# Optimization experiments

Hardware: AMD Instinct MI355X
Metric: run time of the kernel (lower is better)

## Reference

```python
import jax, jax.numpy as jnp
import numpy as np

B, L, D = 8, 8192, 256
H = 4 * D
EPS_LN = 1e-5
EPS_RELU = 1e-6
MIN_A, MAX_A, OFFSET = 0, 3, 3


def setup_inputs() -> dict:
    key = jax.random.key(0)
    ks = jax.random.split(key, 6)
    def n(k, shape, s=0.02):
        return jax.random.normal(k, shape, jnp.float32) * s
    return {
        "x": jax.random.normal(ks[0], (B, L, D), jnp.float32),
        "g1": jnp.ones((D,), jnp.float32), "b1": jnp.zeros((D,), jnp.float32),
        "g2": jnp.ones((D,), jnp.float32), "b2": jnp.zeros((D,), jnp.float32),
        "filt_w": n(ks[1], (L, D)),
        "w1": n(ks[2], (D, H)), "bb1": jnp.zeros((H,), jnp.float32),
        "w2": n(ks[3], (H, D)), "bb2": jnp.zeros((D,), jnp.float32),
    }


def layernorm(x, g, b):
    m = jnp.mean(x, -1, keepdims=True)
    v = jnp.var(x, -1, keepdims=True)
    return (x - m) * jax.lax.rsqrt(v + EPS_LN) * g + b


def maxpool_same(x, w):
    # stride-1 max pool over the last (frequency) axis, SAME padding
    if w == 1:
        return x
    return jax.lax.reduce_window(x, -jnp.inf, jax.lax.max,
                                 (1, 1, w), (1, 1, 1), "SAME")


def spsd1d(xt):
    """SPSD1D: FFT-based multi-scale (alpha) max-pooling spectral filter.
    xt: (B, D, L). Keeps rfft bins that are local maxima at every scale
    2**alpha for alpha in [MIN_A, MAX_A]; the lowest OFFSET bins pass through.
    Returns filtered signal (B, D, L) and argmax-alpha holder (B, D, F)."""
    X = jnp.fft.rfft(xt, axis=-1)              # (B, D, F), F = L//2 + 1
    mag = jnp.abs(X)
    pooled = jnp.stack([maxpool_same(mag, 2 ** a)
                        for a in range(MIN_A, MAX_A + 1)], 0)  # (A, B, D, F)
    max_holder = jnp.argmax(pooled, axis=0)
    env = jnp.max(pooled, axis=0)
    keep = (mag >= env) | (jnp.arange(mag.shape[-1]) < OFFSET)
    Xf = jnp.where(keep, X, 0.0)
    out = jnp.fft.irfft(Xf, n=xt.shape[-1], axis=-1)
    return out, max_holder


def _block_forward(x, g1, b1, g2, b2, filt_w, w1, bb1, w2, bb2):
    # EpsilonReLU(LayerNorm(x))
    h = jax.nn.relu(layernorm(x, g1, b1)) + EPS_RELU      # (B, L, D)
    # GlobalSPSDFilter: spsd over sequence axis, then elementwise weight
    f, _max_holder = spsd1d(jnp.swapaxes(h, 1, 2))        # (B, D, L)
    x0 = jnp.swapaxes(f, 1, 2) * filt_w                   # (B, L, D)
    # MLP(LayerNorm(x0)); dropouts are identity in eval mode
    m = layernorm(x0, g2, b2)
    m = jax.nn.gelu(m @ w1 + bb1, approximate=False)
    x0 = m @ w2 + bb2
    return x + x0


def reference(x, g1, b1, g2, b2, filt_w, w1, bb1, w2, bb2):
    return _block_forward(x, g1, b1, g2, b2, filt_w, w1, bb1, w2, bb2)
```

## Files before the change

kernel.cpp:

```cpp
#include <hip/hip_runtime.h>
#include <hip/hip_bf16.h>

#define BSZ  8
#define LSEQ 8192
#define DDIM 256
#define HDIM 1024
#define MFFT 4096

typedef __bf16 bf16;
typedef __bf16 bf16x8 __attribute__((ext_vector_type(8)));
typedef __bf16 bf16x4 __attribute__((ext_vector_type(4)));
typedef float  f32x4  __attribute__((ext_vector_type(4)));
typedef float  f32x16 __attribute__((ext_vector_type(16)));

__device__ __forceinline__ void wave_reduce2(float& a, float& b) {
    #pragma unroll
    for (int off = 1; off < 64; off <<= 1) {
        a += __shfl_xor(a, off);
        b += __shfl_xor(b, off);
    }
}

__device__ __forceinline__ void gl_lds16(const void* g, void* l) {
    __builtin_amdgcn_global_load_lds(
        (const __attribute__((address_space(1))) unsigned int*)(unsigned long long)g,
        (__attribute__((address_space(3))) unsigned int*)(unsigned int)(unsigned long long)l,
        16, 0, 0);
}

__global__ __launch_bounds__(256) void k0_prep(const float* __restrict__ w1,
                                               const float* __restrict__ w2,
                                               bf16* __restrict__ w1k,
                                               bf16* __restrict__ w2k,
                                               float2* __restrict__ tbl) {
    const int e = blockIdx.x * 256 + threadIdx.x;
    {
        const int c = e >> 14, r = e & 16383;
        const int ks = r >> 11, grp = (r >> 9) & 3, hh = (r >> 3) & 63, j = r & 7;
        w1k[e] = (bf16)w1[(ks * 32 + grp * 8 + j) * HDIM + c * 64 + hh];
    }
    {
        const int c = e >> 14, r = e & 16383;
        const int ks4 = r >> 12, g2 = (r >> 11) & 1, d = (r >> 3) & 255, j = r & 7;
        w2k[e] = (bf16)w2[(c * 64 + ks4 * 16 + g2 * 8 + j) * DDIM + d];
    }
    if (e <= 8184) {
        float ang;
        if (e < 3584) {
            const int f = e / 512 + 1, jj = e & 511;
            ang = -6.283185307179586f * (float)(f * jj) * (1.0f / 4096.0f);
        } else if (e < 4032) {
            const int t = e - 3584, f = t / 64 + 1, jj = t & 63;
            ang = -6.283185307179586f * (float)(f * jj) * (1.0f / 512.0f);
        } else if (e < 4088) {
            const int t = e - 4032, f = t / 8 + 1, jj = t & 7;
            ang = -6.283185307179586f * (float)(f * jj) * (1.0f / 64.0f);
        } else {
            const int k = e - 4088;
            ang = 3.14159265358979323846f * (float)k * (1.0f / 4096.0f);
        }
        tbl[e] = make_float2(cosf(ang), sinf(ang));
    }
}

__global__ __launch_bounds__(256) void k1_ln1_relu_T(const float* __restrict__ x,
                                                     const float* __restrict__ g1,
                                                     const float* __restrict__ b1,
                                                     float* __restrict__ ht) {
    __shared__ float tile[DDIM][33];
    const int tid  = threadIdx.x;
    const int wave = tid >> 6, lane = tid & 63;
    const int b  = blockIdx.x >> 8;
    const int l0 = (blockIdx.x & 255) << 5;
    const float4 g4 = *(const float4*)&g1[lane * 4];
    const float4 b4 = *(const float4*)&b1[lane * 4];
    for (int r8 = 0; r8 < 8; ++r8) {
        const int l = r8 * 4 + wave;
        const float4 v = *(const float4*)&x[(b * LSEQ + l0 + l) * DDIM + lane * 4];
        float s = v.x + v.y + v.z + v.w;
        float q = v.x * v.x + v.y * v.y + v.z * v.z + v.w * v.w;
        wave_reduce2(s, q);
        const float mean = s * (1.0f / 256.0f);
        const float var  = q * (1.0f / 256.0f) - mean * mean;
        const float rstd = rsqrtf(var + 1e-5f);
        const float vv[4] = {v.x, v.y, v.z, v.w};
        const float gg[4] = {g4.x, g4.y, g4.z, g4.w};
        const float bb[4] = {b4.x, b4.y, b4.z, b4.w};
        #pragma unroll
        for (int j = 0; j < 4; ++j) {
            float t = (vv[j] - mean) * rstd * gg[j] + bb[j];
            t = fmaxf(t, 0.0f) + 1e-6f;
            tile[lane * 4 + j][l] = t;
        }
    }
    __syncthreads();
    for (int i = tid; i < DDIM * 32; i += 256) {
        const int d = i >> 5, ll = i & 31;
        ht[(b * DDIM + d) * LSEQ + l0 + ll] = tile[d][ll];
    }
}

__device__ __forceinline__ int zs(int p) { return p ^ ((p >> 4) & 15); }
__device__ __forceinline__ float2 cmulf(float2 a, float2 b) {
    return make_float2(fmaf(a.x, b.x, -a.y * b.y), fmaf(a.x, b.y, a.y * b.x));
}
__device__ __forceinline__ float2 f2add(float2 a, float2 b) { return make_float2(a.x + b.x, a.y + b.y); }
__device__ __forceinline__ float2 f2sub(float2 a, float2 b) { return make_float2(a.x - b.x, a.y - b.y); }
#define CSQ2 0.70710678118654752440f

__device__ __forceinline__ void dft8(float2 a0, float2 a1, float2 a2, float2 a3,
                                     float2 a4, float2 a5, float2 a6, float2 a7,
                                     float2& y0, float2& y1, float2& y2, float2& y3,
                                     float2& y4, float2& y5, float2& y6, float2& y7) {
    const float2 s0 = f2add(a0, a4), s1 = f2add(a1, a5), s2 = f2add(a2, a6), s3 = f2add(a3, a7);
    const float2 d0 = f2sub(a0, a4), d1 = f2sub(a1, a5), d2 = f2sub(a2, a6), d3 = f2sub(a3, a7);
    const float2 d1t = make_float2(CSQ2 * (d1.x + d1.y), CSQ2 * (d1.y - d1.x));
    const float2 d2t = make_float2(d2.y, -d2.x);
    const float2 d3t = make_float2(CSQ2 * (d3.y - d3.x), -CSQ2 * (d3.x + d3.y));
    const float2 u0 = f2add(s0, s2), u1 = f2add(s1, s3);
    const float2 v0 = f2sub(s0, s2);
    const float2 sd = f2sub(s1, s3);
    const float2 v1 = make_float2(sd.y, -sd.x);
    const float2 e0 = f2add(d0, d2t), e1 = f2add(d1t, d3t);
    const float2 f0 = f2sub(d0, d2t);
    const float2 dd = f2sub(d1t, d3t);
    const float2 f1 = make_float2(dd.y, -dd.x);
    y0 = f2add(u0, u1); y4 = f2sub(u0, u1);
    y2 = f2add(v0, v1); y6 = f2sub(v0, v1);
    y1 = f2add(e0, e1); y5 = f2sub(e0, e1);
    y3 = f2add(f0, f1); y7 = f2sub(f0, f1);
}

template<int LQ, int TOFF>
__device__ __forceinline__ void stage8(float2* Z, const float2* __restrict__ tw, int tid) {
    const int q = 1 << LQ;
    const int j = tid & (q - 1);
    const int base = ((tid >> LQ) << (LQ + 3)) + j;
    const float2 a0 = Z[zs(base)],         a1 = Z[zs(base + q)];
    const float2 a2 = Z[zs(base + 2 * q)], a3 = Z[zs(base + 3 * q)];
    const float2 a4 = Z[zs(base + 4 * q)], a5 = Z[zs(base + 5 * q)];
    const float2 a6 = Z[zs(base + 6 * q)], a7 = Z[zs(base + 7 * q)];
    float2 y0, y1, y2, y3, y4, y5, y6, y7;
    dft8(a0, a1, a2, a3, a4, a5, a6, a7, y0, y1, y2, y3, y4, y5, y6, y7);
    y1 = cmulf(y1, tw[TOFF + j]);
    y2 = cmulf(y2, tw[TOFF + q + j]);
    y3 = cmulf(y3, tw[TOFF + 2 * q + j]);
    y4 = cmulf(y4, tw[TOFF + 3 * q + j]);
    y5 = cmulf(y5, tw[TOFF + 4 * q + j]);
    y6 = cmulf(y6, tw[TOFF + 5 * q + j]);
    y7 = cmulf(y7, tw[TOFF + 6 * q + j]);
    Z[zs(base)]         = y0;
    Z[zs(base + 4 * q)] = y1;
    Z[zs(base + 2 * q)] = y2;
    Z[zs(base + 6 * q)] = y3;
    Z[zs(base + q)]     = y4;
    Z[zs(base + 5 * q)] = y5;
    Z[zs(base + 3 * q)] = y6;
    Z[zs(base + 7 * q)] = y7;
    __syncthreads();
}

__device__ __forceinline__ void stage8_last(float2* Z, int tid) {
    const int base = tid << 3;
    const float2 a0 = Z[zs(base)],     a1 = Z[zs(base + 1)];
    const float2 a2 = Z[zs(base + 2)], a3 = Z[zs(base + 3)];
    const float2 a4 = Z[zs(base + 4)], a5 = Z[zs(base + 5)];
    const float2 a6 = Z[zs(base + 6)], a7 = Z[zs(base + 7)];
    __syncthreads();
    float2 y0, y1, y2, y3, y4, y5, y6, y7;
    dft8(a0, a1, a2, a3, a4, a5, a6, a7, y0, y1, y2, y3, y4, y5, y6, y7);
    const int r9 = (int)(__brev((unsigned)tid) >> 23);
    Z[zs(r9)]        = y0;
    Z[zs(512 + r9)]  = y1;
    Z[zs(1024 + r9)] = y2;
    Z[zs(1536 + r9)] = y3;
    Z[zs(2048 + r9)] = y4;
    Z[zs(2560 + r9)] = y5;
    Z[zs(3072 + r9)] = y6;
    Z[zs(3584 + r9)] = y7;
    __syncthreads();
}

__device__ __forceinline__ void fft4096(float2* Z, const float2* __restrict__ tw, int tid) {
    stage8<9, 0>(Z, tw, tid);
    stage8<6, 3584>(Z, tw, tid);
    stage8<3, 4032>(Z, tw, tid);
    stage8_last(Z, tid);
}

__global__ __launch_bounds__(512, 4) void k2_spsd(float* __restrict__ ht,
                                                  const float2* __restrict__ tw) {
    __shared__ float2 Z[MFFT];
    __shared__ float  mg[MFFT + 1];
    const int tid = threadIdx.x;
    float* row = ht + (size_t)blockIdx.x * LSEQ;
    const float2* U = tw + 4088;

    for (int m = tid; m < MFFT; m += 512)
        Z[zs(m)] = *(const float2*)&row[2 * m];
    __syncthreads();

    fft4096(Z, tw, tid);

    for (int k = tid; k <= MFFT; k += 512) {
        const int ka = k & (MFFT - 1);
        const int kb = (MFFT - k) & (MFFT - 1);
        const float2 A = Z[zs(ka)], Bc = Z[zs(kb)];
        const float zex = 0.5f * (A.x + Bc.x), zey = 0.5f * (A.y - Bc.y);
        const float zox = 0.5f * (A.y + Bc.y), zoy = -0.5f * (A.x - Bc.x);
        const float2 u = U[k];
        const float cs = u.x, sn = -u.y;
        const float xr = zex + zox * cs - zoy * sn;
        const float xi = zey + zox * sn + zoy * cs;
        mg[k] = sqrtf(xr * xr + xi * xi);
    }
    __syncthreads();

    for (int k = tid; k <= 2048; k += 512) {
        const int km = (MFFT - k) & (MFFT - 1);
        const float2 Pk = Z[zs(k)];
        const float2 Pm = Z[zs(km)];
        const float2 u = U[k];
        const float cs = u.x, sn = u.y;
        const float zex = 0.5f * (Pk.x + Pm.x), zey = 0.5f * (Pk.y - Pm.y);
        const float zox = 0.5f * (Pk.y + Pm.y), zoy = -0.5f * (Pk.x - Pm.x);
        float xkr = zex + zox * cs + zoy * sn;
        float xki = zey - zox * sn + zoy * cs;
        const float zex2 = 0.5f * (Pm.x + Pk.x), zey2 = 0.5f * (Pm.y - Pk.y);
        const float zox2 = 0.5f * (Pm.y + Pk.y), zoy2 = -0.5f * (Pm.x - Pk.x);
        float xmr = zex2 - zox2 * cs + zoy2 * sn;
        float xmi = zey2 - zox2 * sn - zoy2 * cs;
        const int jm = MFFT - k;
        bool keepk, keepm;
        {
            const int lo = (k - 3 < 0) ? 0 : k - 3;
            const int hi = (k + 4 > 4096) ? 4096 : k + 4;
            float mx = mg[k];
            for (int t2 = lo; t2 <= hi; ++t2) mx = fmaxf(mx, mg[t2]);
            keepk = (k < 3) || (mg[k] >= mx);
        }
        {
            const int hi = (jm + 4 > 4096) ? 4096 : jm + 4;
            float mx = mg[jm];
            for (int t2 = jm - 3; t2 <= hi; ++t2) mx = fmaxf(mx, mg[t2]);
            keepm = (mg[jm] >= mx);
        }
        if (!keepk) { xkr = 0.0f; xki = 0.0f; }
        if (!keepm) { xmr = 0.0f; xmi = 0.0f; }
        const float zpex = 0.5f * (xkr + xmr), zpey = 0.5f * (xki - xmi);
        const float dfx  = 0.5f * (xkr - xmr), dfy  = 0.5f * (xki + xmi);
        const float zpox = dfx * cs - dfy * sn, zpoy = dfx * sn + dfy * cs;
        const float2 zk = make_float2(zpex - zpoy, zpey + zpox);
        const float zex3 = 0.5f * (xmr + xkr), zey3 = 0.5f * (xmi - xki);
        const float df2x = 0.5f * (xmr - xkr), df2y = 0.5f * (xmi + xki);
        const float zo3x = -df2x * cs - df2y * sn, zo3y = df2x * sn - df2y * cs;
        const float2 zm = make_float2(zex3 - zo3y, zey3 + zo3x);
        Z[zs(k)] = make_float2(zk.x, -zk.y);
        if (k != 0 && k != 2048) Z[zs(MFFT - k)] = make_float2(zm.x, -zm.y);
    }
    __syncthreads();

    fft4096(Z, tw, tid);

    const float invM = 1.0f / (float)MFFT;
    for (int m = tid; m < MFFT; m += 512) {
        const float2 z = Z[zs(m)];
        *(float2*)&row[2 * m] = make_float2(z.x * invM, -z.y * invM);
    }
}

__global__ __launch_bounds__(256) void k3_filt_ln2(const float* __restrict__ ht,
                                                   const float* __restrict__ fw,
                                                   const float* __restrict__ g2,
                                                   const float* __restrict__ b2,
                                                   bf16* __restrict__ aln) {
    __shared__ float tile[DDIM][33];
    const int tid  = threadIdx.x;
    const int wave = tid >> 6, lane = tid & 63;
    const int b  = blockIdx.x >> 8;
    const int l0 = (blockIdx.x & 255) << 5;
    for (int i = tid; i < DDIM * 32; i += 256) {
        const int d = i >> 5, ll = i & 31;
        tile[d][ll] = ht[(b * DDIM + d) * LSEQ + l0 + ll];
    }
    __syncthreads();
    const float4 g4 = *(const float4*)&g2[lane * 4];
    const float4 bb4 = *(const float4*)&b2[lane * 4];
    for (int r8 = 0; r8 < 8; ++r8) {
        const int l = r8 * 4 + wave;
        const int gl = l0 + l;
        const float4 f4 = *(const float4*)&fw[gl * DDIM + lane * 4];
        float v[4];
        v[0] = tile[lane * 4 + 0][l] * f4.x;
        v[1] = tile[lane * 4 + 1][l] * f4.y;
        v[2] = tile[lane * 4 + 2][l] * f4.z;
        v[3] = tile[lane * 4 + 3][l] * f4.w;
        float s = v[0] + v[1] + v[2] + v[3];
        float q = v[0] * v[0] + v[1] * v[1] + v[2] * v[2] + v[3] * v[3];
        wave_reduce2(s, q);
        const float mean = s * (1.0f / 256.0f);
        const float var  = q * (1.0f / 256.0f) - mean * mean;
        const float rstd = rsqrtf(var + 1e-5f);
        const float gg[4] = {g4.x, g4.y, g4.z, g4.w};
        const float bb[4] = {bb4.x, bb4.y, bb4.z, bb4.w};
        bf16x4 o;
        #pragma unroll
        for (int j = 0; j < 4; ++j)
            o[j] = (bf16)((v[j] - mean) * rstd * gg[j] + bb[j]);
        *(bf16x4*)&aln[(b * LSEQ + gl) * DDIM + lane * 4] = o;
    }
}

#define LDS_W1 0
#define LDS_W2 32768
#define LDS_LM 65536
#define LDS_TOT 73728

#define MFMA16 __builtin_amdgcn_mfma_f32_16x16x32_bf16
#define MFMA32 __builtin_amdgcn_mfma_f32_32x32x16_bf16

__global__ __launch_bounds__(512, 4) void k4_mlp(const bf16* __restrict__ aln,
                                                 const bf16* __restrict__ w1k,
                                                 const bf16* __restrict__ w2k,
                                                 const float* __restrict__ bb1,
                                                 const float* __restrict__ bb2,
                                                 const float* __restrict__ x,
                                                 float* __restrict__ out) {
    extern __shared__ char sm[];
    const int tid = threadIdx.x;
    const int lane = tid & 63, w = tid >> 6;
    const int rowLane = lane & 15, grp = lane >> 4;
    const int wm1 = w >> 1, wn1 = w & 1;
    const int wm2 = w >> 2, wn2 = w & 3;
    const int lane32 = lane & 31, g2l = lane >> 5;
    const int row0 = blockIdx.x << 6;

    bf16x8 aF[8];
    {
        const size_t rb = (size_t)(row0 + wm1 * 16 + rowLane) * DDIM;
        #pragma unroll
        for (int ks = 0; ks < 8; ++ks)
            aF[ks] = *(const bf16x8*)(aln + rb + ks * 32 + grp * 8);
    }
    {
        const char* g1 = (const char*)w1k;
        #pragma unroll
        for (int r = 0; r < 4; ++r)
            gl_lds16(g1 + r * 8192 + tid * 16, sm + LDS_W1 + r * 8192 + tid * 16);
    }
    __syncthreads();

    f32x16 acc0 = {0.f}, acc1 = {0.f};
    #pragma unroll
    for (int i = 0; i < 16; ++i) { acc0[i] = 0.f; acc1[i] = 0.f; }

    for (int c = 0; c < 16; ++c) {
        {
            const char* g2p = (const char*)w2k + (size_t)c * 32768;
            #pragma unroll
            for (int r = 0; r < 4; ++r)
                gl_lds16(g2p + r * 8192 + tid * 16, sm + LDS_W2 + r * 8192 + tid * 16);
        }
        const int hc0 = wn1 * 32 + rowLane;

        f32x4 p0 = {0.f, 0.f, 0.f, 0.f}, p1 = p0;
        #pragma unroll
        for (int ks = 0; ks < 8; ++ks) {
            const bf16x8 b0 = *(const bf16x8*)(sm + LDS_W1 + ks * 4096 + grp * 1024 + hc0 * 16);
            const bf16x8 b1 = *(const bf16x8*)(sm + LDS_W1 + ks * 4096 + grp * 1024 + (hc0 + 16) * 16);
            p0 = MFMA16(aF[ks], b0, p0, 0, 0, 0);
            p1 = MFMA16(aF[ks], b1, p1, 0, 0, 0);
        }
        {
            const float bias0 = bb1[c * 64 + hc0];
            const float bias1 = bb1[c * 64 + hc0 + 16];
            const int hc1 = hc0 + 16;
            const int base0 = (((hc0 >> 4) * 2 + ((hc0 >> 3) & 1)) * 64) * 16 + (hc0 & 7) * 2;
            const int base1 = (((hc1 >> 4) * 2 + ((hc1 >> 3) & 1)) * 64) * 16 + (hc1 & 7) * 2;
            #pragma unroll
            for (int j = 0; j < 4; ++j) {
                const int prow = wm1 * 16 + grp * 4 + j;
                const float v0 = p0[j] + bias0;
                const float ge0 = 0.5f * v0 * (1.0f + erff(v0 * 0.70710678118654752f));
                *(bf16*)(sm + LDS_LM + base0 + prow * 16) = (bf16)ge0;
                const float v1 = p1[j] + bias1;
                const float ge1 = 0.5f * v1 * (1.0f + erff(v1 * 0.70710678118654752f));
                *(bf16*)(sm + LDS_LM + base1 + prow * 16) = (bf16)ge1;
            }
        }
        __syncthreads();
        if (c < 15) {
            const char* g1 = (const char*)w1k + (size_t)(c + 1) * 32768;
            #pragma unroll
            for (int r = 0; r < 4; ++r)
                gl_lds16(g1 + r * 8192 + tid * 16, sm + LDS_W1 + r * 8192 + tid * 16);
        }
        #pragma unroll
        for (int ks4 = 0; ks4 < 4; ++ks4) {
            const int plane = (ks4 * 2 + g2l);
            const bf16x8 aM = *(const bf16x8*)(sm + LDS_LM + (plane * 64 + wm2 * 32 + lane32) * 16);
            const bf16x8 bw0 = *(const bf16x8*)(sm + LDS_W2 + (plane * 256 + wn2 * 64 + lane32) * 16);
            const bf16x8 bw1 = *(const bf16x8*)(sm + LDS_W2 + (plane * 256 + wn2 * 64 + 32 + lane32) * 16);
            acc0 = MFMA32(aM, bw0, acc0, 0, 0, 0);
            acc1 = MFMA32(aM, bw1, acc1, 0, 0, 0);
        }
        __syncthreads();
    }
    #pragma unroll
    for (int fn = 0; fn < 2; ++fn) {
        const int dcol = wn2 * 64 + fn * 32 + lane32;
        const float b2v = bb2[dcol];
        #pragma unroll
        for (int reg = 0; reg < 16; ++reg) {
            const int orow = row0 + wm2 * 32 + (reg & 3) + 8 * (reg >> 2) + 4 * g2l;
            const int gi = orow * DDIM + dcol;
            const float a = fn ? acc1[reg] : acc0[reg];
            out[gi] = a + b2v + x[gi];
        }
    }
}

extern "C" void kernel_launch(void* const* d_in, const int* in_sizes, int n_in,
                              void* d_out, int out_size, void* d_ws, size_t ws_size,
                              hipStream_t stream) {
    (void)in_sizes; (void)n_in; (void)out_size; (void)ws_size;
    const float* x   = (const float*)d_in[0];
    const float* g1  = (const float*)d_in[1];
    const float* b1  = (const float*)d_in[2];
    const float* g2  = (const float*)d_in[3];
    const float* b2  = (const float*)d_in[4];
    const float* fw  = (const float*)d_in[5];
    const float* w1  = (const float*)d_in[6];
    const float* bb1 = (const float*)d_in[7];
    const float* w2  = (const float*)d_in[8];
    const float* bb2 = (const float*)d_in[9];
    float* out = (float*)d_out;
    char*  ws  = (char*)d_ws;

    bf16*   aln = (bf16*)ws;
    bf16*   w1k = (bf16*)(ws + (size_t)33554432);
    bf16*   w2k = (bf16*)(ws + (size_t)34078720);
    float2* tbl = (float2*)(ws + (size_t)34603008);
    float* ht = out;

    k0_prep<<<dim3(1024), dim3(256), 0, stream>>>(w1, w2, w1k, w2k, tbl);
    k1_ln1_relu_T<<<dim3(2048), dim3(256), 0, stream>>>(x, g1, b1, ht);
    k2_spsd<<<dim3(2048), dim3(512), 0, stream>>>(ht, tbl);
    k3_filt_ln2<<<dim3(2048), dim3(256), 0, stream>>>(ht, fw, g2, b2, aln);
    k4_mlp<<<dim3(1024), dim3(512), LDS_TOT, stream>>>(aln, w1k, w2k, bb1, bb2, x, out);
}
```

Before: 245.5 us.

## Fuse global load into first FFT stage and merge spectrum post-processing passes

The first radix-8 FFT stage now reads its inputs straight from global memory instead of staging the row into LDS and syncing first. The separate magnitude pass is merged into the real-to-complex split pass. That pass computes the full spectrum once, stores it back into Z and writes squared magnitudes, so sqrt is dropped because only comparisons use it. The filtering pass then reads the precomputed spectrum. This removes an LDS round trip, a barrier and duplicate split arithmetic, but needs an extra barrier and relies on squared magnitudes keeping the same ordering.

```diff
diff --git a/kernel.cpp b/kernel.cpp
--- a/kernel.cpp
+++ b/kernel.cpp
@@ -160,6 +160,37 @@
     __syncthreads();
 }
 
+__device__ __forceinline__ void stage8_first_global(float2* Z, const float2* __restrict__ tw,
+                                                    int tid, const float* __restrict__ row) {
+    const int j = tid;
+    const float2 a0 = *(const float2*)&row[2 * j];
+    const float2 a1 = *(const float2*)&row[2 * (j + 512)];
+    const float2 a2 = *(const float2*)&row[2 * (j + 1024)];
+    const float2 a3 = *(const float2*)&row[2 * (j + 1536)];
+    const float2 a4 = *(const float2*)&row[2 * (j + 2048)];
+    const float2 a5 = *(const float2*)&row[2 * (j + 2560)];
+    const float2 a6 = *(const float2*)&row[2 * (j + 3072)];
+    const float2 a7 = *(const float2*)&row[2 * (j + 3584)];
+    float2 y0, y1, y2, y3, y4, y5, y6, y7;
+    dft8(a0, a1, a2, a3, a4, a5, a6, a7, y0, y1, y2, y3, y4, y5, y6, y7);
+    y1 = cmulf(y1, tw[j]);
+    y2 = cmulf(y2, tw[512 + j]);
+    y3 = cmulf(y3, tw[1024 + j]);
+    y4 = cmulf(y4, tw[1536 + j]);
+    y5 = cmulf(y5, tw[2048 + j]);
+    y6 = cmulf(y6, tw[2560 + j]);
+    y7 = cmulf(y7, tw[3072 + j]);
+    Z[zs(j)]        = y0;
+    Z[zs(j + 2048)] = y1;
+    Z[zs(j + 1024)] = y2;
+    Z[zs(j + 3072)] = y3;
+    Z[zs(j + 512)]  = y4;
+    Z[zs(j + 2560)] = y5;
+    Z[zs(j + 1536)] = y6;
+    Z[zs(j + 3584)] = y7;
+    __syncthreads();
+}
+
 __device__ __forceinline__ void stage8_last(float2* Z, int tid) {
     const int base = tid << 3;
     const float2 a0 = Z[zs(base)],     a1 = Z[zs(base + 1)];
@@ -181,6 +212,14 @@
     __syncthreads();
 }
 
+__device__ __forceinline__ void fft4096_fwd(float2* Z, const float2* __restrict__ tw,
+                                            int tid, const float* __restrict__ row) {
+    stage8_first_global(Z, tw, tid, row);
+    stage8<6, 3584>(Z, tw, tid);
+    stage8<3, 4032>(Z, tw, tid);
+    stage8_last(Z, tid);
+}
+
 __device__ __forceinline__ void fft4096(float2* Z, const float2* __restrict__ tw, int tid) {
     stage8<9, 0>(Z, tw, tid);
     stage8<6, 3584>(Z, tw, tid);
@@ -196,25 +235,7 @@
     float* row = ht + (size_t)blockIdx.x * LSEQ;
     const float2* U = tw + 4088;
 
-    for (int m = tid; m < MFFT; m += 512)
-        Z[zs(m)] = *(const float2*)&row[2 * m];
-    __syncthreads();
-
-    fft4096(Z, tw, tid);
-
-    for (int k = tid; k <= MFFT; k += 512) {
-        const int ka = k & (MFFT - 1);
-        const int kb = (MFFT - k) & (MFFT - 1);
-        const float2 A = Z[zs(ka)], Bc = Z[zs(kb)];
-        const float zex = 0.5f * (A.x + Bc.x), zey = 0.5f * (A.y - Bc.y);
-        const float zox = 0.5f * (A.y + Bc.y), zoy = -0.5f * (A.x - Bc.x);
-        const float2 u = U[k];
-        const float cs = u.x, sn = -u.y;
-        const float xr = zex + zox * cs - zoy * sn;
-        const float xi = zey + zox * sn + zoy * cs;
-        mg[k] = sqrtf(xr * xr + xi * xi);
-    }
-    __syncthreads();
+    fft4096_fwd(Z, tw, tid, row);
 
     for (int k = tid; k <= 2048; k += 512) {
         const int km = (MFFT - k) & (MFFT - 1);
@@ -224,12 +245,34 @@
         const float cs = u.x, sn = u.y;
         const float zex = 0.5f * (Pk.x + Pm.x), zey = 0.5f * (Pk.y - Pm.y);
         const float zox = 0.5f * (Pk.y + Pm.y), zoy = -0.5f * (Pk.x - Pm.x);
-        float xkr = zex + zox * cs + zoy * sn;
-        float xki = zey - zox * sn + zoy * cs;
-        const float zex2 = 0.5f * (Pm.x + Pk.x), zey2 = 0.5f * (Pm.y - Pk.y);
-        const float zox2 = 0.5f * (Pm.y + Pk.y), zoy2 = -0.5f * (Pm.x - Pk.x);
-        float xmr = zex2 - zox2 * cs + zoy2 * sn;
-        float xmi = zey2 - zox2 * sn - zoy2 * cs;
+        const float xkr = zex + zox * cs + zoy * sn;
+        const float xki = zey - zox * sn + zoy * cs;
+        const float xmr = zex - zox * cs - zoy * sn;
+        const float xmi = -zey - zox * sn + zoy * cs;
+        mg[k]        = xkr * xkr + xki * xki;
+        mg[MFFT - k] = xmr * xmr + xmi * xmi;
+        if (k == 0) {
+            Z[zs(0)] = make_float2(xkr, xmr);
+        } else {
+            Z[zs(k)]  = make_float2(xkr, xki);
+            Z[zs(km)] = make_float2(xmr, xmi);
+        }
+    }
+    __syncthreads();
+
+    for (int k = tid; k <= 2048; k += 512) {
+        const int km = (MFFT - k) & (MFFT - 1);
+        float xkr, xki, xmr, xmi;
+        if (k == 0) {
+            const float2 v = Z[zs(0)];
+            xkr = v.x; xki = 0.0f; xmr = v.y; xmi = 0.0f;
+        } else {
+            const float2 a = Z[zs(k)];
+            const float2 b = Z[zs(km)];
+            xkr = a.x; xki = a.y; xmr = b.x; xmi = b.y;
+        }
+        const float2 u = U[k];
+        const float cs = u.x, sn = u.y;
         const int jm = MFFT - k;
         bool keepk, keepm;
         {
@@ -350,7 +393,7 @@
     }
     __syncthreads();
 
-    f32x16 acc0 = {0.f}, acc1 = {0.f};
+    f32x16 acc0, acc1;
     #pragma unroll
     for (int i = 0; i < 16; ++i) { acc0[i] = 0.f; acc1[i] = 0.f; }
 
```

After: 234.6 us (median of 2 runs). 1.05x faster.
